# Performance work log

Measured on AMD Instinct MI355X. Metric: run time of the kernel, lower is better.

The kernel has to match this reference:

```python
import jax, jax.numpy as jnp
import numpy as np

WINDOW_SIZE = 11
SIGMA = 1.5
DATA_RANGE = 1.0
C1 = (0.01 * DATA_RANGE) ** 2
C2 = (0.03 * DATA_RANGE) ** 2


def _gaussian_window(size: int, sigma: float) -> jnp.ndarray:
    coords = jnp.arange(size, dtype=jnp.float32) - size // 2
    g = jnp.exp(-(coords ** 2) / (2.0 * sigma ** 2))
    g = g / g.sum()
    w2d = g[:, None] * g[None, :]
    return w2d[None, None, :, :]  # (O=1, I=1, K, K)


def _conv_same(x, window):
    pad = WINDOW_SIZE // 2
    return jax.lax.conv_general_dilated(
        x, window,
        window_strides=(1, 1),
        padding=((pad, pad), (pad, pad)),
        dimension_numbers=("NCHW", "OIHW", "NCHW"),
    )


def setup_inputs() -> dict:
    key = jax.random.key(0)
    kx, ky = jax.random.split(key)
    B, C, H, W = 64, 1, 512, 512
    x = jax.random.uniform(kx, (B, C, H, W), dtype=jnp.float32)
    y = jax.random.uniform(ky, (B, C, H, W), dtype=jnp.float32)
    return {"x": x, "y": y}


def reference(x, y):
    window = _gaussian_window(WINDOW_SIZE, SIGMA)
    mu_x = _conv_same(x, window)
    mu_y = _conv_same(y, window)
    mu_x_sq = mu_x * mu_x
    mu_y_sq = mu_y * mu_y
    mu_xy = mu_x * mu_y
    sigma_x_sq = _conv_same(x * x, window) - mu_x_sq
    sigma_y_sq = _conv_same(y * y, window) - mu_y_sq
    sigma_xy = _conv_same(x * y, window) - mu_xy
    num = (2.0 * mu_xy + C1) * (2.0 * sigma_xy + C2)
    den = (mu_x_sq + mu_y_sq + C1) * (sigma_x_sq + sigma_y_sq + C2)
    ssim_map = num / den
    ssim_val = ssim_map.mean(axis=(1, 2, 3))  # (B,)
    loss = 1.0 - ssim_val
    return loss.mean()  # reduction='mean'
```

## Files before the change

kernel.cpp:

```cpp
#include <hip/hip_runtime.h>
#include <hip/hip_fp16.h>

typedef _Float16 f16x8 __attribute__((ext_vector_type(8)));
typedef float    f32x4 __attribute__((ext_vector_type(4)));

#define IMG   512
#define NIMG  64
#define TS_R  32
#define TS_C  64
#define NBLK  (NIMG * (IMG/TS_R) * (IMG/TS_C))
#define XST   88
#define HTS   40
#define SROWS 42
#define NU    840

#define C1F   1.0e-4f
#define C2F   9.0e-4f
#define INVSUM 0.26601174f

__device__ __forceinline__ uint2 cvt4h(f32x4 a) {
    __half2 p0 = __floats2half2_rn(a[0], a[1]);
    __half2 p1 = __floats2half2_rn(a[2], a[3]);
    uint2 r; r.x = *reinterpret_cast<uint*>(&p0); r.y = *reinterpret_cast<uint*>(&p1);
    return r;
}

__global__ __launch_bounds__(256, 4)
void ssim_main(const float* __restrict__ x, const float* __restrict__ y,
               float* __restrict__ partial) {
    __shared__ __align__(16) __half XYp[2 * SROWS * XST];
    __shared__ __align__(16) __half Ht[5][TS_C][HTS];
    __shared__ float red[4];

    const int tid  = threadIdx.x;
    const int lane = tid & 63;
    const int wv   = tid >> 6;
    const int l16  = lane & 15;
    const int g16  = lane >> 4;
    const int n0   = wv * 16;

    const int img = blockIdx.z;
    const int r0  = blockIdx.y * TS_R;
    const int c0  = blockIdx.x * TS_C;
    const float* xb = x + (size_t)img * IMG * IMG;
    const float* yb = y + (size_t)img * IMG * IMG;

    float4 st[7];
    int    dst_[7];
    {
        int row_u = tid / 20;
        int c4    = tid - row_u * 20;
        #pragma unroll
        for (int i = 0; i < 7; ++i) {
            bool valid = (i < 6) | (tid < 144);
            bool ya  = row_u >= SROWS;
            int  rp  = ya ? row_u - SROWS : row_u;
            int  gr  = r0 - 5 + rp;
            int  gc  = c0 - 8 + c4 * 4;
            bool ok  = valid & ((unsigned)gr < (unsigned)IMG) & ((unsigned)gc < (unsigned)IMG);
            const float* src = (ya ? yb : xb) + (size_t)gr * IMG + gc;
            st[i]   = ok ? *(const float4*)src : make_float4(0.f, 0.f, 0.f, 0.f);
            dst_[i] = row_u * XST + c4 * 4;
            c4 += 16;
            int inc = 12;
            if (c4 >= 20) { c4 -= 20; inc = 13; }
            row_u += inc;
        }
    }

    const int d0 = g16 * 8 - l16 - 3;
    _Float16 bv[11];
    #pragma unroll
    for (int j = 0; j < 11; ++j) {
        int d = d0 + j;
        float t = (float)(d - 5);
        float v = __expf(-t * t * (1.0f / 4.5f)) * INVSUM;
        bv[j] = ((unsigned)d <= 10u) ? (_Float16)v : (_Float16)0.0f;
    }
    f16x8 WhB, WvA;
    #pragma unroll
    for (int j = 0; j < 8; ++j) WhB[j] = bv[j];
    #pragma unroll
    for (int j = 0; j < 8; ++j) WvA[j] = bv[j + 3];

    #pragma unroll
    for (int i = 0; i < 7; ++i) {
        if (i < 6 || tid < 144) {
            __half2 p0 = __floats2half2_rn(st[i].x, st[i].y);
            __half2 p1 = __floats2half2_rn(st[i].z, st[i].w);
            uint2 v; v.x = *reinterpret_cast<uint*>(&p0); v.y = *reinterpret_cast<uint*>(&p1);
            *(uint2*)&XYp[dst_[i]] = v;
        }
    }
    __syncthreads();

    const int hcol = n0 + l16;
    float ssum = 0.0f;

    auto hpass = [&](int mg, int sb) {
        int srow = mg * 16 + l16;
        if (srow > SROWS - 1) srow = SROWS - 1;
        int off = srow * XST + n0 + g16 * 8;
        f16x8 xf = *(const f16x8*)&XYp[off];
        f16x8 yf = *(const f16x8*)&XYp[SROWS * XST + off];
        f16x8 xx = xf * xf;
        f16x8 yy = yf * yf;
        f16x8 xy = xf * yf;
        f32x4 z = {0.f, 0.f, 0.f, 0.f};
        f32x4 aX  = __builtin_amdgcn_mfma_f32_16x16x32_f16(xf, WhB, z, 0, 0, 0);
        f32x4 aY  = __builtin_amdgcn_mfma_f32_16x16x32_f16(yf, WhB, z, 0, 0, 0);
        f32x4 aXX = __builtin_amdgcn_mfma_f32_16x16x32_f16(xx, WhB, z, 0, 0, 0);
        f32x4 aYY = __builtin_amdgcn_mfma_f32_16x16x32_f16(yy, WhB, z, 0, 0, 0);
        f32x4 aXY = __builtin_amdgcn_mfma_f32_16x16x32_f16(xy, WhB, z, 0, 0, 0);
        int hrow = sb + g16 * 4;
        *(uint2*)&Ht[0][hcol][hrow] = cvt4h(aX);
        *(uint2*)&Ht[1][hcol][hrow] = cvt4h(aY);
        *(uint2*)&Ht[2][hcol][hrow] = cvt4h(aXX);
        *(uint2*)&Ht[3][hcol][hrow] = cvt4h(aYY);
        *(uint2*)&Ht[4][hcol][hrow] = cvt4h(aXY);
    };

    auto vpass = [&](int mt) {
        int ko = (mt * 16 + g16 * 8) & 31;
        f16x8 b0 = *(const f16x8*)&Ht[0][hcol][ko];
        f16x8 b1 = *(const f16x8*)&Ht[1][hcol][ko];
        f16x8 b2 = *(const f16x8*)&Ht[2][hcol][ko];
        f16x8 b3 = *(const f16x8*)&Ht[3][hcol][ko];
        f16x8 b4 = *(const f16x8*)&Ht[4][hcol][ko];
        f32x4 z = {0.f, 0.f, 0.f, 0.f};
        f32x4 cX  = __builtin_amdgcn_mfma_f32_16x16x32_f16(WvA, b0, z, 0, 0, 0);
        f32x4 cY  = __builtin_amdgcn_mfma_f32_16x16x32_f16(WvA, b1, z, 0, 0, 0);
        f32x4 cXX = __builtin_amdgcn_mfma_f32_16x16x32_f16(WvA, b2, z, 0, 0, 0);
        f32x4 cYY = __builtin_amdgcn_mfma_f32_16x16x32_f16(WvA, b3, z, 0, 0, 0);
        f32x4 cXY = __builtin_amdgcn_mfma_f32_16x16x32_f16(WvA, b4, z, 0, 0, 0);
        #pragma unroll
        for (int r = 0; r < 4; ++r) {
            float mx  = cX[r];
            float my  = cY[r];
            float exx = cXX[r];
            float eyy = cYY[r];
            float exy = cXY[r];
            float mxx = mx * mx, myy = my * my, mxy = mx * my;
            float vx  = exx - mxx;
            float vy  = eyy - myy;
            float vxy = exy - mxy;
            float num = (2.0f * mxy + C1F) * (2.0f * vxy + C2F);
            float den = (mxx + myy + C1F) * (vx + vy + C2F);
            ssum = fmaf(num, __builtin_amdgcn_rcpf(den), ssum);
        }
    };

    hpass(0, 0);
    hpass(1, 16);
    vpass(0);
    hpass(2, 0);
    vpass(1);

    #pragma unroll
    for (int off = 32; off > 0; off >>= 1)
        ssum += __shfl_down(ssum, off, 64);
    if ((tid & 63) == 0) red[tid >> 6] = ssum;
    __syncthreads();
    if (tid == 0) {
        float tot = red[0] + red[1] + red[2] + red[3];
        int bi = (blockIdx.z * gridDim.y + blockIdx.y) * gridDim.x + blockIdx.x;
        partial[bi] = tot;
    }
}

__global__ __launch_bounds__(1024)
void ssim_final(const float* __restrict__ partial, float* __restrict__ out) {
    __shared__ float red[16];
    float s = 0.0f;
    for (int i = threadIdx.x; i < NBLK; i += 1024) s += partial[i];
    #pragma unroll
    for (int off = 32; off > 0; off >>= 1)
        s += __shfl_down(s, off, 64);
    if ((threadIdx.x & 63) == 0) red[threadIdx.x >> 6] = s;
    __syncthreads();
    if (threadIdx.x == 0) {
        float tot = 0.0f;
        #pragma unroll
        for (int i = 0; i < 16; ++i) tot += red[i];
        out[0] = 1.0f - tot * (1.0f / 16777216.0f);
    }
}

extern "C" void kernel_launch(void* const* d_in, const int* in_sizes, int n_in,
                              void* d_out, int out_size, void* d_ws, size_t ws_size,
                              hipStream_t stream) {
    const float* x = (const float*)d_in[0];
    const float* y = (const float*)d_in[1];
    float* out     = (float*)d_out;
    float* partial = (float*)d_ws;

    dim3 grid(IMG / TS_C, IMG / TS_R, NIMG);
    ssim_main<<<grid, 256, 0, stream>>>(x, y, partial);
    ssim_final<<<1, 1024, 0, stream>>>(partial, out);
}
```

Measured before the change: 55.62 us.

## Double tile height to 64 rows and pack SSIM epilogue math into float2

Doubles the row tile from 32 to 64, so each block loads a 74-row halo instead of 42 and runs two more horizontal/vertical MFMA pass pairs. This cuts the fraction of redundant halo loads and halves the block count. The epilogue is rewritten with 2-wide float vectors so the compiler can emit packed FP32 ops. The cost is more registers (12 float4 staging loads), more shared memory, and a lower occupancy hint (3 blocks per CU instead of 4).

```diff
diff --git a/kernel.cpp b/kernel.cpp
--- a/kernel.cpp
+++ b/kernel.cpp
@@ -3,16 +3,17 @@
 
 typedef _Float16 f16x8 __attribute__((ext_vector_type(8)));
 typedef float    f32x4 __attribute__((ext_vector_type(4)));
+typedef float    f32x2 __attribute__((ext_vector_type(2)));
 
 #define IMG   512
 #define NIMG  64
-#define TS_R  32
+#define TS_R  64
 #define TS_C  64
 #define NBLK  (NIMG * (IMG/TS_R) * (IMG/TS_C))
 #define XST   88
 #define HTS   40
-#define SROWS 42
-#define NU    840
+#define SROWS 74
+#define UNITS (2 * SROWS * 20)
 
 #define C1F   1.0e-4f
 #define C2F   9.0e-4f
@@ -25,7 +26,7 @@
     return r;
 }
 
-__global__ __launch_bounds__(256, 4)
+__global__ __launch_bounds__(256, 3)
 void ssim_main(const float* __restrict__ x, const float* __restrict__ y,
                float* __restrict__ partial) {
     __shared__ __align__(16) __half XYp[2 * SROWS * XST];
@@ -45,22 +46,20 @@
     const float* xb = x + (size_t)img * IMG * IMG;
     const float* yb = y + (size_t)img * IMG * IMG;
 
-    float4 st[7];
-    int    dst_[7];
+    float4 st[12];
     {
         int row_u = tid / 20;
         int c4    = tid - row_u * 20;
         #pragma unroll
-        for (int i = 0; i < 7; ++i) {
-            bool valid = (i < 6) | (tid < 144);
+        for (int i = 0; i < 12; ++i) {
+            bool valid = (i < 11) | (tid < UNITS - 11 * 256);
             bool ya  = row_u >= SROWS;
             int  rp  = ya ? row_u - SROWS : row_u;
             int  gr  = r0 - 5 + rp;
             int  gc  = c0 - 8 + c4 * 4;
             bool ok  = valid & ((unsigned)gr < (unsigned)IMG) & ((unsigned)gc < (unsigned)IMG);
             const float* src = (ya ? yb : xb) + (size_t)gr * IMG + gc;
-            st[i]   = ok ? *(const float4*)src : make_float4(0.f, 0.f, 0.f, 0.f);
-            dst_[i] = row_u * XST + c4 * 4;
+            st[i] = ok ? *(const float4*)src : make_float4(0.f, 0.f, 0.f, 0.f);
             c4 += 16;
             int inc = 12;
             if (c4 >= 20) { c4 -= 20; inc = 13; }
@@ -83,22 +82,30 @@
     #pragma unroll
     for (int j = 0; j < 8; ++j) WvA[j] = bv[j + 3];
 
-    #pragma unroll
-    for (int i = 0; i < 7; ++i) {
-        if (i < 6 || tid < 144) {
-            __half2 p0 = __floats2half2_rn(st[i].x, st[i].y);
-            __half2 p1 = __floats2half2_rn(st[i].z, st[i].w);
-            uint2 v; v.x = *reinterpret_cast<uint*>(&p0); v.y = *reinterpret_cast<uint*>(&p1);
-            *(uint2*)&XYp[dst_[i]] = v;
+    {
+        int row_u = tid / 20;
+        int c4    = tid - row_u * 20;
+        #pragma unroll
+        for (int i = 0; i < 12; ++i) {
+            if (i < 11 || tid < UNITS - 11 * 256) {
+                __half2 p0 = __floats2half2_rn(st[i].x, st[i].y);
+                __half2 p1 = __floats2half2_rn(st[i].z, st[i].w);
+                uint2 v; v.x = *reinterpret_cast<uint*>(&p0); v.y = *reinterpret_cast<uint*>(&p1);
+                *(uint2*)&XYp[row_u * XST + c4 * 4] = v;
+            }
+            c4 += 16;
+            int inc = 12;
+            if (c4 >= 20) { c4 -= 20; inc = 13; }
+            row_u += inc;
         }
     }
     __syncthreads();
 
     const int hcol = n0 + l16;
-    float ssum = 0.0f;
-
-    auto hpass = [&](int mg, int sb) {
-        int srow = mg * 16 + l16;
+    f32x2 ssum2 = {0.0f, 0.0f};
+
+    auto hpass = [&](int g, int sb) {
+        int srow = g * 16 + l16;
         if (srow > SROWS - 1) srow = SROWS - 1;
         int off = srow * XST + n0 + g16 * 8;
         f16x8 xf = *(const f16x8*)&XYp[off];
@@ -134,19 +141,22 @@
         f32x4 cYY = __builtin_amdgcn_mfma_f32_16x16x32_f16(WvA, b3, z, 0, 0, 0);
         f32x4 cXY = __builtin_amdgcn_mfma_f32_16x16x32_f16(WvA, b4, z, 0, 0, 0);
         #pragma unroll
-        for (int r = 0; r < 4; ++r) {
-            float mx  = cX[r];
-            float my  = cY[r];
-            float exx = cXX[r];
-            float eyy = cYY[r];
-            float exy = cXY[r];
-            float mxx = mx * mx, myy = my * my, mxy = mx * my;
-            float vx  = exx - mxx;
-            float vy  = eyy - myy;
-            float vxy = exy - mxy;
-            float num = (2.0f * mxy + C1F) * (2.0f * vxy + C2F);
-            float den = (mxx + myy + C1F) * (vx + vy + C2F);
-            ssum = fmaf(num, __builtin_amdgcn_rcpf(den), ssum);
+        for (int h = 0; h < 2; ++h) {
+            f32x2 mx  = {cX [2*h], cX [2*h+1]};
+            f32x2 my  = {cY [2*h], cY [2*h+1]};
+            f32x2 exx = {cXX[2*h], cXX[2*h+1]};
+            f32x2 eyy = {cYY[2*h], cYY[2*h+1]};
+            f32x2 exy = {cXY[2*h], cXY[2*h+1]};
+            f32x2 mxx = mx * mx, myy = my * my, mxy = mx * my;
+            f32x2 vx  = exx - mxx;
+            f32x2 vy  = eyy - myy;
+            f32x2 vxy = exy - mxy;
+            f32x2 num = (2.0f * mxy + C1F) * (2.0f * vxy + C2F);
+            f32x2 den = (mxx + myy + C1F) * (vx + vy + C2F);
+            f32x2 r;
+            r[0] = __builtin_amdgcn_rcpf(den[0]);
+            r[1] = __builtin_amdgcn_rcpf(den[1]);
+            ssum2 += num * r;
         }
     };
 
@@ -155,7 +165,12 @@
     vpass(0);
     hpass(2, 0);
     vpass(1);
-
+    hpass(3, 16);
+    vpass(2);
+    hpass(4, 0);
+    vpass(3);
+
+    float ssum = ssum2[0] + ssum2[1];
     #pragma unroll
     for (int off = 32; off > 0; off >>= 1)
         ssum += __shfl_down(ssum, off, 64);
```

Measured after the change: 56.83 us. 1.02x slower.
